# Kernel optimization log

Hardware: AMD Instinct MI355X
Metric: run time of the kernel (lower is better)

Reference implementation:

```python
import jax, jax.numpy as jnp
import numpy as np

B, S, P, C = 128, 672, 168, 500  # batch, seq_len, pred_len, channels

def setup_inputs() -> dict:
    key = jax.random.key(0)
    k1, k2, k3 = jax.random.split(key, 3)
    x = jax.random.normal(k1, (B, S, C), dtype=jnp.float32)
    # per-channel Linear(seq_len -> pred_len): W[c] is [pred_len, seq_len], b[c] is [pred_len]
    W = jax.random.normal(k2, (C, P, S), dtype=jnp.float32) * (1.0 / np.sqrt(S))
    b = jax.random.normal(k3, (C, P), dtype=jnp.float32) * (1.0 / np.sqrt(S))
    return {"x": x, "W": W, "b": b}

def reference(x, W, b):
    # NLinear: subtract last time step, per-channel linear over time, add back
    seq_last = x[:, -1:, :]                     # [B, 1, C]
    xc = x - seq_last                           # [B, S, C]
    # batched over channels: out[b,p,c] = sum_s xc[b,s,c] * W[c,p,s] + b[c,p]
    out = jnp.einsum('bsc,cps->bpc', xc, W) + b.T[None, :, :]
    return out + seq_last
```

## Files before the change

### kernel.cpp

```cpp
#include <hip/hip_runtime.h>


typedef __attribute__((ext_vector_type(8))) short short8;
typedef __attribute__((ext_vector_type(4))) float floatx4;

namespace {
constexpr int Bn = 128, Sn = 672, Pn = 168, Cn = 500;
constexpr int XQ = Bn * Sn;
constexpr int TC = 64, TS = 96, TROW = TS + 12;
constexpr int NS  = Sn / 32;
constexpr int NPT = 11;
constexpr int WROW = 680;
}

__device__ __forceinline__ unsigned short f2bf(float f) {
  unsigned int u = __builtin_bit_cast(unsigned int, f);
  u += 0x7fffu + ((u >> 16) & 1u);
  return (unsigned short)(u >> 16);
}

__global__ __launch_bounds__(256)
void xpose_kernel(const float* __restrict__ x, unsigned short* __restrict__ xq) {
  __shared__ unsigned short T[TC][TROW];
  const int b  = blockIdx.x;
  const int s0 = blockIdx.y * TS;
  const int c0 = blockIdx.z * TC;
  const int t  = threadIdx.x;

  #pragma unroll
  for (int i = 0; i < 6; ++i) {
    const int idx = t + i * 256;
    const int sr  = idx >> 4;
    const int cq  = (idx & 15) * 4;
    int c = c0 + cq;
    if (c > Cn - 4) c = Cn - 4;
    const int rel = c - c0;
    const float4 xv = *(const float4*)&x[(size_t)(b * Sn + s0 + sr) * Cn + c];
    const float4 xl = *(const float4*)&x[(size_t)(b * Sn + (Sn - 1)) * Cn + c];
    T[rel + 0][sr] = f2bf(xv.x - xl.x);
    T[rel + 1][sr] = f2bf(xv.y - xl.y);
    T[rel + 2][sr] = f2bf(xv.z - xl.z);
    T[rel + 3][sr] = f2bf(xv.w - xl.w);
  }
  __syncthreads();
  #pragma unroll
  for (int i = 0; i < 6; ++i) {
    const int idx = t + i * 256;
    const int cr  = idx / 24;
    const int sq  = (idx % 24) * 4;
    const int c   = c0 + cr;
    if (c >= Cn) continue;
    const ushort4 v = *(const ushort4*)&T[cr][sq];
    *(ushort4*)&xq[(size_t)c * XQ + b * Sn + s0 + sq] = v;
  }
}

#define BAR_LGKM() asm volatile("s_waitcnt lgkmcnt(0)\n\ts_barrier" ::: "memory")

__global__ __launch_bounds__(512, 2)
void gemm_kernel(const unsigned short* __restrict__ xq, const float* __restrict__ W,
                 const float* __restrict__ bias, const float* __restrict__ x,
                 float* __restrict__ out) {
  __shared__ unsigned short Wl[2][16 * WROW];
  __shared__ float xl_l[Bn];
  __shared__ float bi_l[Pn];

  const int bid = blockIdx.x;
  const int xcd = bid & 7, sub = bid >> 3;
  const int c0  = xcd * 62 + (xcd < 4 ? xcd : 4) + sub;

  const int tid  = threadIdx.x;
  const int lane = tid & 63;
  const int wv   = tid >> 6;
  const int r16  = lane & 15;
  const int kg   = lane >> 4;

  int wrow[6], wcol[6];
  #pragma unroll
  for (int k = 0; k < 6; ++k) {
    const int f = tid + 512 * k;
    wrow[k] = f / 168;
    wcol[k] = f % 168;
  }
  const bool w5 = tid < 128;
  float4 wreg[6];

  auto loadW = [&](int pt) {
    #pragma unroll
    for (int k = 0; k < 6; ++k) {
      if (k == 5 && !w5) continue;
      int row = pt * 16 + wrow[k];
      if (row > Pn - 1) row = Pn - 1;
      wreg[k] = *(const float4*)&W[((size_t)c0 * Pn + row) * Sn + wcol[k] * 4];
    }
  };
  auto writeW = [&](int buf) {
    #pragma unroll
    for (int k = 0; k < 6; ++k) {
      if (k == 5 && !w5) continue;
      ushort4 u;
      u.x = f2bf(wreg[k].x); u.y = f2bf(wreg[k].y);
      u.z = f2bf(wreg[k].z); u.w = f2bf(wreg[k].w);
      *(ushort4*)&Wl[buf][wrow[k] * WROW + wcol[k] * 4] = u;
    }
  };

  loadW(0);

  if (tid < Bn) xl_l[tid] = x[((size_t)tid * Sn + (Sn - 1)) * Cn + c0];
  else if (tid < Bn + Pn) bi_l[tid - Bn] = bias[(size_t)c0 * Pn + (tid - Bn)];

  const unsigned short* aBase = xq + (size_t)c0 * XQ + (wv * 16 + r16) * Sn + kg * 8;
  short8 aR[NS];
  #pragma unroll
  for (int s = 0; s < NS; ++s) aR[s] = *(const short8*)(aBase + s * 32);

  writeW(0);
  loadW(1);
  BAR_LGKM();

  #pragma unroll 1
  for (int pt = 0; pt < NPT; ++pt) {
    const int buf = pt & 1;

    if (pt + 1 < NPT) {
      writeW(buf ^ 1);
      if (pt + 2 < NPT) loadW(pt + 2);
    }

    floatx4 acc = (floatx4){0.f, 0.f, 0.f, 0.f};
    const int rdb = r16 * WROW + kg * 8;
    #pragma unroll
    for (int s = 0; s < NS; ++s) {
      const short8 wf = *(const short8*)&Wl[buf][rdb + s * 32];
      acc = __builtin_amdgcn_mfma_f32_16x16x32_bf16(aR[s], wf, acc, 0, 0, 0);
    }

    const int p = pt * 16 + r16;
    if (p < Pn) {
      const float bi = bi_l[p];
      #pragma unroll
      for (int r = 0; r < 4; ++r) {
        const int b = wv * 16 + kg * 4 + r;
        out[((size_t)b * Pn + p) * Cn + c0] = acc[r] + bi + xl_l[b];
      }
    }

    if (pt + 1 < NPT) BAR_LGKM();
  }
}

extern "C" void kernel_launch(void* const* d_in, const int* in_sizes, int n_in,
                              void* d_out, int out_size, void* d_ws, size_t ws_size,
                              hipStream_t stream) {
  (void)in_sizes; (void)n_in; (void)out_size; (void)ws_size;
  const float* x  = (const float*)d_in[0];
  const float* W  = (const float*)d_in[1];
  const float* bv = (const float*)d_in[2];
  float* out = (float*)d_out;
  unsigned short* xq = (unsigned short*)d_ws;

  hipLaunchKernelGGL(xpose_kernel, dim3(Bn, Sn / TS, (Cn + TC - 1) / TC), dim3(256), 0, stream,
                     x, xq);
  hipLaunchKernelGGL(gemm_kernel, dim3(Cn), dim3(512), 0, stream,
                     xq, W, bv, x, out);
}
```

Measured before the change: 161.0 us.

## Split GEMM blocks by batch half and simplify W staging pipeline

Each channel's work is split across two 256-thread blocks, each handling 64 batch rows, giving 1000 blocks with a 3-per-CU occupancy hint. W tiles are staged with a direct load-convert-store into the next LDS buffer rather than a register-held two-stage prefetch, and the LDS row pitch changes from 680 to 676. The aim is better CU occupancy and load balance. The cost is that each channel's W is now read and converted twice, and the prefetch is shallower.

```diff
diff --git a/kernel.cpp b/kernel.cpp
--- a/kernel.cpp
+++ b/kernel.cpp
@@ -10,7 +10,7 @@
 constexpr int TC = 64, TS = 96, TROW = TS + 12;
 constexpr int NS  = Sn / 32;
 constexpr int NPT = 11;
-constexpr int WROW = 680;
+constexpr int WROW = 676;
 }
 
 __device__ __forceinline__ unsigned short f2bf(float f) {
@@ -57,17 +57,18 @@
 
 #define BAR_LGKM() asm volatile("s_waitcnt lgkmcnt(0)\n\ts_barrier" ::: "memory")
 
-__global__ __launch_bounds__(512, 2)
+__global__ __launch_bounds__(256, 3)
 void gemm_kernel(const unsigned short* __restrict__ xq, const float* __restrict__ W,
                  const float* __restrict__ bias, const float* __restrict__ x,
                  float* __restrict__ out) {
   __shared__ unsigned short Wl[2][16 * WROW];
-  __shared__ float xl_l[Bn];
+  __shared__ float xl_l[64];
   __shared__ float bi_l[Pn];
 
   const int bid = blockIdx.x;
-  const int xcd = bid & 7, sub = bid >> 3;
-  const int c0  = xcd * 62 + (xcd < 4 ? xcd : 4) + sub;
+  const int wid = (bid & 7) * 125 + (bid >> 3);
+  const int c0  = wid >> 1;
+  const int bh  = wid & 1;
 
   const int tid  = threadIdx.x;
   const int lane = tid & 63;
@@ -75,58 +76,42 @@
   const int r16  = lane & 15;
   const int kg   = lane >> 4;
 
-  int wrow[6], wcol[6];
-  #pragma unroll
-  for (int k = 0; k < 6; ++k) {
-    const int f = tid + 512 * k;
-    wrow[k] = f / 168;
-    wcol[k] = f % 168;
-  }
-  const bool w5 = tid < 128;
-  float4 wreg[6];
+  const float* Wc = W + (size_t)c0 * Pn * Sn;
 
-  auto loadW = [&](int pt) {
+  auto stageW = [&](int pt, int buf) {
     #pragma unroll
-    for (int k = 0; k < 6; ++k) {
-      if (k == 5 && !w5) continue;
-      int row = pt * 16 + wrow[k];
-      if (row > Pn - 1) row = Pn - 1;
-      wreg[k] = *(const float4*)&W[((size_t)c0 * Pn + row) * Sn + wcol[k] * 4];
-    }
-  };
-  auto writeW = [&](int buf) {
-    #pragma unroll
-    for (int k = 0; k < 6; ++k) {
-      if (k == 5 && !w5) continue;
+    for (int k = 0; k < 11; ++k) {
+      if (k == 10 && tid >= 128) continue;
+      const int idx  = tid + 256 * k;
+      const int row  = idx / 168;
+      const int colw = idx * 4 - row * 672;
+      int p = pt * 16 + row;
+      if (p > Pn - 1) p = Pn - 1;
+      const float4 w = *(const float4*)(Wc + (size_t)p * Sn + colw);
       ushort4 u;
-      u.x = f2bf(wreg[k].x); u.y = f2bf(wreg[k].y);
-      u.z = f2bf(wreg[k].z); u.w = f2bf(wreg[k].w);
-      *(ushort4*)&Wl[buf][wrow[k] * WROW + wcol[k] * 4] = u;
+      u.x = f2bf(w.x); u.y = f2bf(w.y); u.z = f2bf(w.z); u.w = f2bf(w.w);
+      *(ushort4*)&Wl[buf][row * WROW + colw] = u;
     }
   };
 
-  loadW(0);
-
-  if (tid < Bn) xl_l[tid] = x[((size_t)tid * Sn + (Sn - 1)) * Cn + c0];
-  else if (tid < Bn + Pn) bi_l[tid - Bn] = bias[(size_t)c0 * Pn + (tid - Bn)];
-
-  const unsigned short* aBase = xq + (size_t)c0 * XQ + (wv * 16 + r16) * Sn + kg * 8;
+  stageW(0, 0);
+  if (tid < 64) {
+    const int b = bh * 64 + tid;
+    xl_l[tid] = x[((size_t)b * Sn + (Sn - 1)) * Cn + c0];
+  } else if (tid < 64 + Pn) {
+    bi_l[tid - 64] = bias[(size_t)c0 * Pn + (tid - 64)];
+  }
+  const unsigned short* aBase =
+      xq + (size_t)c0 * XQ + (size_t)(bh * 64 + wv * 16 + r16) * Sn + kg * 8;
   short8 aR[NS];
   #pragma unroll
   for (int s = 0; s < NS; ++s) aR[s] = *(const short8*)(aBase + s * 32);
-
-  writeW(0);
-  loadW(1);
   BAR_LGKM();
 
   #pragma unroll 1
   for (int pt = 0; pt < NPT; ++pt) {
     const int buf = pt & 1;
-
-    if (pt + 1 < NPT) {
-      writeW(buf ^ 1);
-      if (pt + 2 < NPT) loadW(pt + 2);
-    }
+    if (pt + 1 < NPT) stageW(pt + 1, buf ^ 1);
 
     floatx4 acc = (floatx4){0.f, 0.f, 0.f, 0.f};
     const int rdb = r16 * WROW + kg * 8;
@@ -141,8 +126,8 @@
       const float bi = bi_l[p];
       #pragma unroll
       for (int r = 0; r < 4; ++r) {
-        const int b = wv * 16 + kg * 4 + r;
-        out[((size_t)b * Pn + p) * Cn + c0] = acc[r] + bi + xl_l[b];
+        const int bl = wv * 16 + kg * 4 + r;
+        out[((size_t)(bh * 64 + bl) * Pn + p) * Cn + c0] = acc[r] + bi + xl_l[bl];
       }
     }
 
@@ -162,6 +147,6 @@
 
   hipLaunchKernelGGL(xpose_kernel, dim3(Bn, Sn / TS, (Cn + TC - 1) / TC), dim3(256), 0, stream,
                      x, xq);
-  hipLaunchKernelGGL(gemm_kernel, dim3(Cn), dim3(512), 0, stream,
+  hipLaunchKernelGGL(gemm_kernel, dim3(1000), dim3(256), 0, stream,
                      xq, W, bv, x, out);
 }
```

Result: slower. 235.4 us (+46.2%).

## Restructure GEMM to stream K-chunks of X through LDS with W held in registers

Applied to the files above, without the earlier changes.

The per-channel GEMM now gives each of 11 waves a fixed 16-row slice of the prediction dimension. It streams the reduction dimension in 32-wide steps, double-buffering bf16 X tiles through LDS, and loads and converts W directly from global memory into registers. Each wave keeps 8 accumulators covering all batch rows. This replaces staging all of W in LDS and keeping the X fragments in registers, reducing LDS footprint and reordering data reuse. The costs are 704-thread blocks at one block per CU, a barrier on every K step, and W fetched with fine-grained per-lane loads.

```diff
diff --git a/kernel.cpp b/kernel.cpp
--- a/kernel.cpp
+++ b/kernel.cpp
@@ -9,8 +9,7 @@
 constexpr int XQ = Bn * Sn;
 constexpr int TC = 64, TS = 96, TROW = TS + 12;
 constexpr int NS  = Sn / 32;
-constexpr int NPT = 11;
-constexpr int WROW = 680;
+constexpr int APITCH = 40;
 }
 
 __device__ __forceinline__ unsigned short f2bf(float f) {
@@ -57,13 +56,12 @@
 
 #define BAR_LGKM() asm volatile("s_waitcnt lgkmcnt(0)\n\ts_barrier" ::: "memory")
 
-__global__ __launch_bounds__(512, 2)
+__global__ __launch_bounds__(704, 1)
 void gemm_kernel(const unsigned short* __restrict__ xq, const float* __restrict__ W,
                  const float* __restrict__ bias, const float* __restrict__ x,
                  float* __restrict__ out) {
-  __shared__ unsigned short Wl[2][16 * WROW];
+  __shared__ unsigned short Al[2][Bn * APITCH];
   __shared__ float xl_l[Bn];
-  __shared__ float bi_l[Pn];
 
   const int bid = blockIdx.x;
   const int xcd = bid & 7, sub = bid >> 3;
@@ -75,78 +73,92 @@
   const int r16  = lane & 15;
   const int kg   = lane >> 4;
 
-  int wrow[6], wcol[6];
+  const bool aDo = tid < 512;
+  const int  ab  = (tid >> 2) & 127;
+  const int  aoct = tid & 3;
+  const unsigned short* aSrc = xq + (size_t)c0 * XQ + ab * Sn + aoct * 8;
+  const int aDst = ab * APITCH + aoct * 8;
+
+  const int p   = wv * 16 + r16;
+  const int pcl = p < Pn ? p : Pn - 1;
+  const float* wSrc = W + ((size_t)c0 * Pn + pcl) * Sn + kg * 8;
+  const float bi = bias[(size_t)c0 * Pn + pcl];
+
+  if (tid < Bn) xl_l[tid] = x[((size_t)tid * Sn + (Sn - 1)) * Cn + c0];
+
+  floatx4 acc[8];
   #pragma unroll
-  for (int k = 0; k < 6; ++k) {
-    const int f = tid + 512 * k;
-    wrow[k] = f / 168;
-    wcol[k] = f % 168;
-  }
-  const bool w5 = tid < 128;
-  float4 wreg[6];
+  for (int bs = 0; bs < 8; ++bs) acc[bs] = (floatx4){0.f, 0.f, 0.f, 0.f};
 
-  auto loadW = [&](int pt) {
+  short8 a0, a1;
+  float4 wA0, wB0, wA1, wB1;
+
+  auto lA0 = [&](int s) { if (aDo) a0 = *(const short8*)(aSrc + s * 32); };
+  auto lA1 = [&](int s) { if (aDo) a1 = *(const short8*)(aSrc + s * 32); };
+  auto lW0 = [&](int s) {
+    wA0 = *(const float4*)(wSrc + s * 32);
+    wB0 = *(const float4*)(wSrc + s * 32 + 4);
+  };
+  auto lW1 = [&](int s) {
+    wA1 = *(const float4*)(wSrc + s * 32);
+    wB1 = *(const float4*)(wSrc + s * 32 + 4);
+  };
+  auto wrA0 = [&](int buf) { if (aDo) *(short8*)&Al[buf][aDst] = a0; };
+  auto wrA1 = [&](int buf) { if (aDo) *(short8*)&Al[buf][aDst] = a1; };
+
+  auto comp0 = [&](int buf, int nextS, bool reload) {
+    short8 wb;
+    wb[0] = (short)f2bf(wA0.x); wb[1] = (short)f2bf(wA0.y);
+    wb[2] = (short)f2bf(wA0.z); wb[3] = (short)f2bf(wA0.w);
+    wb[4] = (short)f2bf(wB0.x); wb[5] = (short)f2bf(wB0.y);
+    wb[6] = (short)f2bf(wB0.z); wb[7] = (short)f2bf(wB0.w);
+    if (reload) lW0(nextS);
     #pragma unroll
-    for (int k = 0; k < 6; ++k) {
-      if (k == 5 && !w5) continue;
-      int row = pt * 16 + wrow[k];
-      if (row > Pn - 1) row = Pn - 1;
-      wreg[k] = *(const float4*)&W[((size_t)c0 * Pn + row) * Sn + wcol[k] * 4];
+    for (int bs = 0; bs < 8; ++bs) {
+      const short8 af = *(const short8*)&Al[buf][(bs * 16 + r16) * APITCH + kg * 8];
+      acc[bs] = __builtin_amdgcn_mfma_f32_16x16x32_bf16(af, wb, acc[bs], 0, 0, 0);
     }
   };
-  auto writeW = [&](int buf) {
+  auto comp1 = [&](int buf, int nextS, bool reload) {
+    short8 wb;
+    wb[0] = (short)f2bf(wA1.x); wb[1] = (short)f2bf(wA1.y);
+    wb[2] = (short)f2bf(wA1.z); wb[3] = (short)f2bf(wA1.w);
+    wb[4] = (short)f2bf(wB1.x); wb[5] = (short)f2bf(wB1.y);
+    wb[6] = (short)f2bf(wB1.z); wb[7] = (short)f2bf(wB1.w);
+    if (reload) lW1(nextS);
     #pragma unroll
-    for (int k = 0; k < 6; ++k) {
-      if (k == 5 && !w5) continue;
-      ushort4 u;
-      u.x = f2bf(wreg[k].x); u.y = f2bf(wreg[k].y);
-      u.z = f2bf(wreg[k].z); u.w = f2bf(wreg[k].w);
-      *(ushort4*)&Wl[buf][wrow[k] * WROW + wcol[k] * 4] = u;
+    for (int bs = 0; bs < 8; ++bs) {
+      const short8 af = *(const short8*)&Al[buf][(bs * 16 + r16) * APITCH + kg * 8];
+      acc[bs] = __builtin_amdgcn_mfma_f32_16x16x32_bf16(af, wb, acc[bs], 0, 0, 0);
     }
   };
 
-  loadW(0);
-
-  if (tid < Bn) xl_l[tid] = x[((size_t)tid * Sn + (Sn - 1)) * Cn + c0];
-  else if (tid < Bn + Pn) bi_l[tid - Bn] = bias[(size_t)c0 * Pn + (tid - Bn)];
-
-  const unsigned short* aBase = xq + (size_t)c0 * XQ + (wv * 16 + r16) * Sn + kg * 8;
-  short8 aR[NS];
-  #pragma unroll
-  for (int s = 0; s < NS; ++s) aR[s] = *(const short8*)(aBase + s * 32);
-
-  writeW(0);
-  loadW(1);
+  lA0(0); lW0(0); lA1(1); lW1(1);
+  wrA0(0);
   BAR_LGKM();
 
   #pragma unroll 1
-  for (int pt = 0; pt < NPT; ++pt) {
-    const int buf = pt & 1;
+  for (int jj = 0; jj < NS - 1; jj += 2) {
+    lA0(jj + 2);
+    wrA1(1);
+    comp0(0, jj + 2, true);
+    BAR_LGKM();
+    if (jj + 3 < NS) lA1(jj + 3);
+    wrA0(0);
+    comp1(1, jj + 3, jj + 3 < NS);
+    BAR_LGKM();
+  }
+  comp0(0, 0, false);
 
-    if (pt + 1 < NPT) {
-      writeW(buf ^ 1);
-      if (pt + 2 < NPT) loadW(pt + 2);
-    }
-
-    floatx4 acc = (floatx4){0.f, 0.f, 0.f, 0.f};
-    const int rdb = r16 * WROW + kg * 8;
+  if (p < Pn) {
     #pragma unroll
-    for (int s = 0; s < NS; ++s) {
-      const short8 wf = *(const short8*)&Wl[buf][rdb + s * 32];
-      acc = __builtin_amdgcn_mfma_f32_16x16x32_bf16(aR[s], wf, acc, 0, 0, 0);
-    }
-
-    const int p = pt * 16 + r16;
-    if (p < Pn) {
-      const float bi = bi_l[p];
+    for (int bs = 0; bs < 8; ++bs) {
       #pragma unroll
       for (int r = 0; r < 4; ++r) {
-        const int b = wv * 16 + kg * 4 + r;
-        out[((size_t)b * Pn + p) * Cn + c0] = acc[r] + bi + xl_l[b];
+        const int b = bs * 16 + kg * 4 + r;
+        out[((size_t)b * Pn + p) * Cn + c0] = acc[bs][r] + bi + xl_l[b];
       }
     }
-
-    if (pt + 1 < NPT) BAR_LGKM();
   }
 }
 
@@ -162,6 +174,6 @@
 
   hipLaunchKernelGGL(xpose_kernel, dim3(Bn, Sn / TS, (Cn + TC - 1) / TC), dim3(256), 0, stream,
                      x, xq);
-  hipLaunchKernelGGL(gemm_kernel, dim3(Cn), dim3(512), 0, stream,
+  hipLaunchKernelGGL(gemm_kernel, dim3(Cn), dim3(704), 0, stream,
                      xq, W, bv, x, out);
 }
```

New measurement: 171.6 us. +6.5%, slower.
